# Optimization experiments

Measured on AMD Instinct MI355X. Metric: run time of the kernel, lower is better.

## Reference

```python
import jax, jax.numpy as jnp
import numpy as np

T, B, N, D, H = 12, 32, 64, 2, 128
HID, HEAD = 32, 4          # GATBlock n_hid, n_head; HEAD*HID == H
M = N * (N - 1)            # edge rows per get_graph
N_ACT = N - 1              # active nodes per batch row


def _make_graph():
    rec = np.zeros((M, N), np.float32)
    snd = np.zeros((M, N), np.float32)
    k = np.arange(N_ACT * N_ACT)
    ii = np.repeat(np.arange(N_ACT), N_ACT)
    jj = np.tile(np.arange(N_ACT), N_ACT)
    snd[k, ii] = 1.0
    rec[k, jj] = 1.0
    return rec, snd


def setup_inputs() -> dict:
    key = jax.random.key(0)
    ks = jax.random.split(key, 16)
    rec, snd = _make_graph()
    inp = {
        "inputs": jax.random.normal(ks[0], (T, B, N, D), jnp.float32),
        "hidden": jax.random.normal(ks[1], (B, N, H), jnp.float32),
        "rel_rec": jnp.asarray(np.broadcast_to(rec, (B, M, N)).copy()),
        "rel_send": jnp.asarray(np.broadcast_to(snd, (B, M, N)).copy()),
        # GATBlock rn1: fc1(D->HID), fc2(2*HID->HEAD)
        "rn1_W1": jax.random.normal(ks[2], (HID, D)) * 0.1,
        "rn1_b1": jnp.zeros((HID,)),
        "rn1_W2": jax.random.normal(ks[3], (HEAD, 2 * HID)) * 0.1,
        "rn1_b2": jnp.zeros((HEAD,)),
        # GATBlock rn2: fc1(H->HID), fc2(2*HID->HEAD)
        "rn2_W1": jax.random.normal(ks[4], (HID, H)) * 0.1,
        "rn2_b1": jnp.zeros((HID,)),
        "rn2_W2": jax.random.normal(ks[5], (HEAD, 2 * HID)) * 0.1,
        "rn2_b2": jnp.zeros((HEAD,)),
        # GRUCell(H, H)
        "gru_Wih": jax.random.normal(ks[6], (3 * H, H)) * 0.05,
        "gru_Whh": jax.random.normal(ks[7], (3 * H, H)) * 0.05,
        "gru_bih": jnp.zeros((3 * H,)),
        "gru_bhh": jnp.zeros((3 * H,)),
        # out Linear(H, D)
        "out_W": jax.random.normal(ks[8], (D, H)) * 0.1,
        "out_b": jnp.zeros((D,)),
    }
    return inp


def _gat_block(x_in, rel_rec, rel_send, W1, b1, W2, b2):
    # x_in: B x N x Din
    x = x_in @ W1.T + b1                                   # B,N,HID
    s = jnp.einsum('bmn,bnd->bmd', rel_send, x)            # B,M,HID (senders)
    r = jnp.einsum('bmn,bnd->bmd', rel_rec, x)             # B,M,HID (receivers)
    a = jax.nn.elu(jnp.concatenate([s, r], -1) @ W2.T + b2)  # B,M,HEAD
    # per-receiving-node masked softmax over the edge dim (edge2node)
    m = rel_rec[..., None] > 0                             # B,M,N,1
    logits = jnp.where(m, a[:, :, None, :], -jnp.inf)      # B,M,N,HEAD
    mx = jnp.max(logits, axis=1, keepdims=True)
    mx = jnp.where(jnp.isfinite(mx), mx, 0.0)
    e = jnp.where(m, jnp.exp(logits - mx), 0.0)
    denom = jnp.sum(e, axis=1, keepdims=True)
    att = e / jnp.where(denom > 0, denom, 1.0)             # B,M,N,HEAD
    # weighted scatter-sum: outer(att_edge, sender_feat) summed per node
    out = jnp.einsum('bmnh,bmd->bnhd', att, s)             # B,N,HEAD,HID
    Bn, Nn = x_in.shape[0], x_in.shape[1]
    return jax.nn.elu(out.reshape(Bn, Nn, HEAD * HID))     # B,N,H


def _gru_cell(x, h, Wih, Whh, bih, bhh):
    gi = x @ Wih.T + bih
    gh = h @ Whh.T + bhh
    i_r, i_z, i_n = jnp.split(gi, 3, axis=-1)
    h_r, h_z, h_n = jnp.split(gh, 3, axis=-1)
    r = jax.nn.sigmoid(i_r + h_r)
    z = jax.nn.sigmoid(i_z + h_z)
    n = jnp.tanh(i_n + r * h_n)
    return (1.0 - z) * n + z * h


def reference(inputs, hidden, rel_rec, rel_send,
              rn1_W1, rn1_b1, rn1_W2, rn1_b2,
              rn2_W1, rn2_b1, rn2_W2, rn2_b2,
              gru_Wih, gru_Whh, gru_bih, gru_bhh,
              out_W, out_b):
    def step(h, x_t):
        x = _gat_block(x_t, rel_rec, rel_send, rn1_W1, rn1_b1, rn1_W2, rn1_b2)
        h = _gru_cell(x, h, gru_Wih, gru_Whh, gru_bih, gru_bhh)
        h = _gat_block(h, rel_rec, rel_send, rn2_W1, rn2_b1, rn2_W2, rn2_b2)
        return h, None
    h_final, _ = jax.lax.scan(step, hidden, inputs)
    pred = h_final @ out_W.T + out_b                       # B,N,D
    return pred
```

## Files before the change

kernel.cpp:

```cpp
#include <hip/hip_runtime.h>


#define T_   12
#define B_   32
#define N_   64
#define D_   2
#define H_   128
#define HID_ 32
#define HEAD_ 4
#define NA_  63

__device__ __forceinline__ float eluf(float x){ return x>0.f ? x : expm1f(x); }

#define OFF_H    0u
#define OFF_X1   262144u
#define OFF_PS1  1048576u
#define OFF_PR1  1146880u
#define OFF_XG   1245184u
#define OFF_X2   4390912u
#define OFF_PS2  4456448u
#define OFF_PR2  4464640u
#define OFF_WT   OFF_X1
#define OFF_GI   4472832u
#define WS_NEED_A ((4472832ull + 9437184ull) * 4ull)

__global__ void gat1_fc(const float* __restrict__ inp, const float* __restrict__ W1,
                        const float* __restrict__ b1, const float* __restrict__ W2,
                        const float* __restrict__ b2,
                        float* __restrict__ x1_all, float* __restrict__ ps_all,
                        float* __restrict__ pr_all){
  int grp = blockIdx.x;
  int tid = threadIdx.x;
  __shared__ float sx1[N_*HID_];
  __shared__ float sW1[HID_*D_];
  __shared__ float sb1[HID_];
  __shared__ float sW2[HEAD_*2*HID_];
  __shared__ float sxin[N_*D_];
  if(tid < 64)  sW1[tid] = W1[tid];
  if(tid < 32)  sb1[tid] = b1[tid];
  sW2[tid] = W2[tid];
  if(tid < 128) sxin[tid] = inp[grp*N_*D_ + tid];
  __syncthreads();
  for(int o = tid; o < N_*HID_; o += 256){
    int n = o >> 5, k = o & 31;
    float v = sb1[k] + sxin[n*2]*sW1[k*2] + sxin[n*2+1]*sW1[k*2+1];
    sx1[o] = v;
    x1_all[grp*N_*HID_ + o] = v;
  }
  __syncthreads();
  for(int p = tid; p < N_*8; p += 256){
    int n = p >> 3, q = p & 7, hh = q & 3;
    const float* w  = sW2 + hh*64 + ((q < 4) ? 0 : 32);
    const float* xr = sx1 + n*32;
    float acc = (q < 4) ? b2[hh] : 0.f;
    #pragma unroll
    for(int c = 0; c < 32; c++) acc += xr[c]*w[c];
    if(q < 4) ps_all[grp*N_*HEAD_ + n*4 + hh] = acc;
    else      pr_all[grp*N_*HEAD_ + n*4 + hh] = acc;
  }
}

__global__ void prep_wt(const float* __restrict__ Wih, const float* __restrict__ Whh,
                        float* __restrict__ wtb){
  int idx = blockIdx.x*256 + threadIdx.x;
  int k4 = idx / 768, j = idx - k4*768;
  const float* src = (j < 384) ? (Wih + (size_t)j*H_) : (Whh + (size_t)(j-384)*H_);
  ((float4*)wtb)[idx] = ((const float4*)src)[k4];
}

__global__ __launch_bounds__(128) void gat_att_big(const float* __restrict__ x1,
    const float* __restrict__ ps, const float* __restrict__ pr,
    float* __restrict__ out){
  int blk = blockIdx.x, g = blk >> 1, part = blk & 1, tid = threadIdx.x;
  __shared__ float sX[N_*HID_];
  __shared__ float sPs[N_*HEAD_];
  __shared__ float sPr[N_*HEAD_];
  {
    const float4* xs = (const float4*)(x1 + (size_t)g*(N_*HID_));
    #pragma unroll
    for(int k = 0; k < 4; k++) ((float4*)sX)[tid + 128*k] = xs[tid + 128*k];
    sPs[tid]       = ps[g*(N_*HEAD_) + tid];
    sPs[tid + 128] = ps[g*(N_*HEAD_) + tid + 128];
    sPr[tid]       = pr[g*(N_*HEAD_) + tid];
    sPr[tid + 128] = pr[g*(N_*HEAD_) + tid + 128];
  }
  __syncthreads();
  float* outg = out + (size_t)g*(N_*H_);
  int r = part*128 + tid;
  if(r < NA_*HEAD_){
    int hh = r & 3;
    float prv = sPr[r];
    float tmax = -1e30f;
    for(int i = 0; i < NA_; i++) tmax = fmaxf(tmax, sPs[i*4 + hh]);
    float m = eluf(tmax + prv);
    float4 acc[8];
    #pragma unroll
    for(int k = 0; k < 8; k++) acc[k] = make_float4(0.f,0.f,0.f,0.f);
    float s = 0.f;
    #pragma unroll 3
    for(int i = 0; i < NA_; i++){
      float tt = sPs[i*4 + hh] + prv;
      float v = tt > 0.f ? tt : expm1f(tt);
      float p = expf(v - m);
      s += p;
      const float4* sxp = (const float4*)&sX[i*32];
      #pragma unroll
      for(int k = 0; k < 8; k++){
        float4 xv = sxp[k];
        acc[k].x += p*xv.x; acc[k].y += p*xv.y;
        acc[k].z += p*xv.z; acc[k].w += p*xv.w;
      }
    }
    float inv = 1.f/s;
    float4* orow = (float4*)(outg + (r>>2)*H_ + hh*32);
    #pragma unroll
    for(int k = 0; k < 8; k++){
      float4 o;
      o.x = eluf(acc[k].x*inv); o.y = eluf(acc[k].y*inv);
      o.z = eluf(acc[k].z*inv); o.w = eluf(acc[k].w*inv);
      orow[k] = o;
    }
  } else {
    float4 z4 = make_float4(0.f,0.f,0.f,0.f);
    float4* zrow = (float4*)(outg + NA_*H_);
    for(int k = r - NA_*HEAD_; k < 32; k += 4) zrow[k] = z4;
  }
}

__global__ __launch_bounds__(192) void gi_gemm2(const float* __restrict__ xg,
    const float* __restrict__ wtb, float* __restrict__ gi){
  int tid = threadIdx.x;
  int r0 = blockIdx.x * 8;
  __shared__ __align__(16) float sxg[8][H_];
  for(int i = tid; i < 256; i += 192)
    ((float4*)sxg)[i] = ((const float4*)(xg + (size_t)r0*H_))[i];
  __syncthreads();
  const float4* wt4 = (const float4*)wtb;
  float acc0[8] = {0,0,0,0,0,0,0,0};
  float acc1[8] = {0,0,0,0,0,0,0,0};
  #pragma unroll 4
  for(int k4 = 0; k4 < 32; k4++){
    float4 w0 = wt4[k4*768 + tid];
    float4 w1 = wt4[k4*768 + tid + 192];
    #pragma unroll
    for(int rr = 0; rr < 8; rr++){
      float4 xv = ((const float4*)sxg[rr])[k4];
      acc0[rr] += w0.x*xv.x + w0.y*xv.y + w0.z*xv.z + w0.w*xv.w;
      acc1[rr] += w1.x*xv.x + w1.y*xv.y + w1.z*xv.z + w1.w*xv.w;
    }
  }
  #pragma unroll
  for(int rr = 0; rr < 8; rr++){
    gi[(size_t)(r0+rr)*384 + tid]       = acc0[rr];
    gi[(size_t)(r0+rr)*384 + tid + 192] = acc1[rr];
  }
}

__global__ __launch_bounds__(512) void gru_fc4(
    const float* __restrict__ gi, const float* __restrict__ h,
    const float* __restrict__ wtb,
    const float* __restrict__ bih, const float* __restrict__ bhh,
    const float* __restrict__ W1, const float* __restrict__ b1,
    const float* __restrict__ W2, const float* __restrict__ b2,
    float* __restrict__ x2, float* __restrict__ ps2, float* __restrict__ pr2){
  int tid = threadIdx.x;
  int g0 = blockIdx.x * 8;
  __shared__ __align__(16) float sh[8][H_];
  __shared__ __align__(16) float shn[8][H_];
  __shared__ float sx2[8][HID_];
  if(tid < 256) ((float4*)sh)[tid] = ((const float4*)(h + (size_t)g0*H_))[tid];
  __syncthreads();
  int c = tid & 127, rg = tid >> 7, r0 = rg*2;
  const float4* wt4 = (const float4*)wtb;
  const float4* hp0 = (const float4*)sh[r0];
  const float4* hp1 = (const float4*)sh[r0+1];
  float ahr[2]={0,0}, ahz[2]={0,0}, ahn[2]={0,0};
  #pragma unroll 4
  for(int k4 = 0; k4 < 32; k4++){
    const float4* wk = wt4 + k4*768 + c;
    float4 w3 = wk[384], w4 = wk[512], w5 = wk[640];
    float4 hv0 = hp0[k4], hv1 = hp1[k4];
    ahr[0] += w3.x*hv0.x + w3.y*hv0.y + w3.z*hv0.z + w3.w*hv0.w;
    ahz[0] += w4.x*hv0.x + w4.y*hv0.y + w4.z*hv0.z + w4.w*hv0.w;
    ahn[0] += w5.x*hv0.x + w5.y*hv0.y + w5.z*hv0.z + w5.w*hv0.w;
    ahr[1] += w3.x*hv1.x + w3.y*hv1.y + w3.z*hv1.z + w3.w*hv1.w;
    ahz[1] += w4.x*hv1.x + w4.y*hv1.y + w4.z*hv1.z + w4.w*hv1.w;
    ahn[1] += w5.x*hv1.x + w5.y*hv1.y + w5.z*hv1.z + w5.w*hv1.w;
  }
  float bi_r = bih[c], bi_z = bih[c+H_], bi_n = bih[c+2*H_];
  float bh_r = bhh[c], bh_z = bhh[c+H_], bh_n = bhh[c+2*H_];
  #pragma unroll
  for(int rr = 0; rr < 2; rr++){
    const float* gir = gi + (size_t)(g0+r0+rr)*384;
    float ir  = gir[c]       + bi_r;
    float iz  = gir[c+128]   + bi_z;
    float in_ = gir[c+256]   + bi_n;
    float hr  = ahr[rr]+bh_r, hz = ahz[rr]+bh_z, hn = ahn[rr]+bh_n;
    float rgt = 1.f/(1.f+expf(-(ir+hr)));
    float zgt = 1.f/(1.f+expf(-(iz+hz)));
    float ngt = tanhf(in_ + rgt*hn);
    shn[r0+rr][c] = (1.f-zgt)*ngt + zgt*sh[r0+rr][c];
  }
  __syncthreads();
  if(tid < 256){
    int r = tid >> 5, jc = tid & 31;
    const float4* wrow = (const float4*)(W1 + (size_t)jc*H_);
    const float4* hnr = (const float4*)shn[r];
    float acc = b1[jc];
    #pragma unroll 8
    for(int k4 = 0; k4 < 32; k4++){
      float4 w = wrow[k4], hv = hnr[k4];
      acc += w.x*hv.x + w.y*hv.y + w.z*hv.z + w.w*hv.w;
    }
    sx2[r][jc] = acc;
    x2[(size_t)(g0+r)*HID_ + jc] = acc;
  }
  __syncthreads();
  if(tid < 64){
    int r = tid >> 3, q = tid & 7, hh = q & 3;
    int base = (q < 4) ? 0 : 32;
    float acc = (q < 4) ? b2[hh] : 0.f;
    #pragma unroll
    for(int cc = 0; cc < 32; cc++) acc += sx2[r][cc]*W2[hh*64 + base + cc];
    if(q < 4) ps2[(g0+r)*HEAD_ + hh] = acc;
    else      pr2[(g0+r)*HEAD_ + hh] = acc;
  }
}

__global__ __launch_bounds__(512) void gru_fc3(
    const float* __restrict__ xg, const float* __restrict__ h,
    const float* __restrict__ wtb,
    const float* __restrict__ bih, const float* __restrict__ bhh,
    const float* __restrict__ W1, const float* __restrict__ b1,
    const float* __restrict__ W2, const float* __restrict__ b2,
    float* __restrict__ x2, float* __restrict__ ps2, float* __restrict__ pr2){
  int tid = threadIdx.x;
  int g0 = blockIdx.x * 8;
  __shared__ __align__(16) float sx[8][H_];
  __shared__ __align__(16) float sh[8][H_];
  __shared__ __align__(16) float shn[8][H_];
  __shared__ float sx2[8][HID_];
  if(tid < 256) ((float4*)sx)[tid]     = ((const float4*)(xg + (size_t)g0*H_))[tid];
  else          ((float4*)sh)[tid-256] = ((const float4*)(h  + (size_t)g0*H_))[tid-256];
  __syncthreads();
  int c = tid & 127, rg = tid >> 7, r0 = rg*2;
  const float4* wt4 = (const float4*)wtb;
  const float4* xr0 = (const float4*)sx[r0];
  const float4* xr1 = (const float4*)sx[r0+1];
  const float4* hp0 = (const float4*)sh[r0];
  const float4* hp1 = (const float4*)sh[r0+1];
  float air[2]={0,0}, aiz[2]={0,0}, ain[2]={0,0};
  float ahr[2]={0,0}, ahz[2]={0,0}, ahn[2]={0,0};
  #pragma unroll 2
  for(int k4 = 0; k4 < 32; k4++){
    const float4* wk = wt4 + k4*768 + c;
    float4 w0 = wk[0],   w1 = wk[128], w2 = wk[256];
    float4 w3 = wk[384], w4 = wk[512], w5 = wk[640];
    float4 xv0 = xr0[k4], xv1 = xr1[k4];
    float4 hv0 = hp0[k4], hv1 = hp1[k4];
    air[0] += w0.x*xv0.x + w0.y*xv0.y + w0.z*xv0.z + w0.w*xv0.w;
    aiz[0] += w1.x*xv0.x + w1.y*xv0.y + w1.z*xv0.z + w1.w*xv0.w;
    ain[0] += w2.x*xv0.x + w2.y*xv0.y + w2.z*xv0.z + w2.w*xv0.w;
    ahr[0] += w3.x*hv0.x + w3.y*hv0.y + w3.z*hv0.z + w3.w*hv0.w;
    ahz[0] += w4.x*hv0.x + w4.y*hv0.y + w4.z*hv0.z + w4.w*hv0.w;
    ahn[0] += w5.x*hv0.x + w5.y*hv0.y + w5.z*hv0.z + w5.w*hv0.w;
    air[1] += w0.x*xv1.x + w0.y*xv1.y + w0.z*xv1.z + w0.w*xv1.w;
    aiz[1] += w1.x*xv1.x + w1.y*xv1.y + w1.z*xv1.z + w1.w*xv1.w;
    ain[1] += w2.x*xv1.x + w2.y*xv1.y + w2.z*xv1.z + w2.w*xv1.w;
    ahr[1] += w3.x*hv1.x + w3.y*hv1.y + w3.z*hv1.z + w3.w*hv1.w;
    ahz[1] += w4.x*hv1.x + w4.y*hv1.y + w4.z*hv1.z + w4.w*hv1.w;
    ahn[1] += w5.x*hv1.x + w5.y*hv1.y + w5.z*hv1.z + w5.w*hv1.w;
  }
  float bi_r = bih[c], bi_z = bih[c+H_], bi_n = bih[c+2*H_];
  float bh_r = bhh[c], bh_z = bhh[c+H_], bh_n = bhh[c+2*H_];
  #pragma unroll
  for(int rr = 0; rr < 2; rr++){
    float ir  = air[rr]+bi_r, iz = aiz[rr]+bi_z, in_ = ain[rr]+bi_n;
    float hr  = ahr[rr]+bh_r, hz = ahz[rr]+bh_z, hn  = ahn[rr]+bh_n;
    float rgt = 1.f/(1.f+expf(-(ir+hr)));
    float zgt = 1.f/(1.f+expf(-(iz+hz)));
    float ngt = tanhf(in_ + rgt*hn);
    shn[r0+rr][c] = (1.f-zgt)*ngt + zgt*sh[r0+rr][c];
  }
  __syncthreads();
  if(tid < 256){
    int r = tid >> 5, jc = tid & 31;
    const float4* wrow = (const float4*)(W1 + (size_t)jc*H_);
    const float4* hnr = (const float4*)shn[r];
    float acc = b1[jc];
    #pragma unroll 8
    for(int k4 = 0; k4 < 32; k4++){
      float4 w = wrow[k4], hv = hnr[k4];
      acc += w.x*hv.x + w.y*hv.y + w.z*hv.z + w.w*hv.w;
    }
    sx2[r][jc] = acc;
    x2[(size_t)(g0+r)*HID_ + jc] = acc;
  }
  __syncthreads();
  if(tid < 64){
    int r = tid >> 3, q = tid & 7, hh = q & 3;
    int base = (q < 4) ? 0 : 32;
    float acc = (q < 4) ? b2[hh] : 0.f;
    #pragma unroll
    for(int cc = 0; cc < 32; cc++) acc += sx2[r][cc]*W2[hh*64 + base + cc];
    if(q < 4) ps2[(g0+r)*HEAD_ + hh] = acc;
    else      pr2[(g0+r)*HEAD_ + hh] = acc;
  }
}

__global__ __launch_bounds__(128) void gat_att_sm(const float* __restrict__ x1,
    const float* __restrict__ ps, const float* __restrict__ pr,
    float* __restrict__ out){
  int bid = blockIdx.x;
  int g = bid >> 3, sub = bid & 7, rh = sub >> 2, dq = sub & 3;
  int tid = threadIdx.x;
  __shared__ float sX[N_*HID_];
  __shared__ float sPs[N_*HEAD_];
  __shared__ float sPr[N_*HEAD_];
  {
    const float4* xs = (const float4*)(x1 + (size_t)g*(N_*HID_));
    #pragma unroll
    for(int k = 0; k < 4; k++) ((float4*)sX)[tid + 128*k] = xs[tid + 128*k];
    sPs[tid]       = ps[g*(N_*HEAD_) + tid];
    sPs[tid + 128] = ps[g*(N_*HEAD_) + tid + 128];
    sPr[tid]       = pr[g*(N_*HEAD_) + tid];
    sPr[tid + 128] = pr[g*(N_*HEAD_) + tid + 128];
  }
  __syncthreads();
  float* outg = out + (size_t)g*(N_*H_);
  if(tid < 126){
    int r = rh*126 + tid;
    int hh = r & 3, j = r >> 2;
    float prv = sPr[r];
    float tmax = -1e30f;
    for(int i = 0; i < NA_; i++) tmax = fmaxf(tmax, sPs[i*4 + hh]);
    float m = eluf(tmax + prv);
    float4 a0 = make_float4(0.f,0.f,0.f,0.f), a1 = a0;
    float s = 0.f;
    #pragma unroll 3
    for(int i = 0; i < NA_; i++){
      float tt = sPs[i*4 + hh] + prv;
      float v = tt > 0.f ? tt : expm1f(tt);
      float p = expf(v - m);
      s += p;
      const float4* sxp = (const float4*)&sX[i*32 + dq*8];
      float4 x0 = sxp[0], x1v = sxp[1];
      a0.x += p*x0.x;  a0.y += p*x0.y;  a0.z += p*x0.z;  a0.w += p*x0.w;
      a1.x += p*x1v.x; a1.y += p*x1v.y; a1.z += p*x1v.z; a1.w += p*x1v.w;
    }
    float inv = 1.f/s;
    float4* orow = (float4*)(outg + (size_t)j*H_ + hh*32 + dq*8);
    float4 o0, o1;
    o0.x = eluf(a0.x*inv); o0.y = eluf(a0.y*inv);
    o0.z = eluf(a0.z*inv); o0.w = eluf(a0.w*inv);
    o1.x = eluf(a1.x*inv); o1.y = eluf(a1.y*inv);
    o1.z = eluf(a1.z*inv); o1.w = eluf(a1.w*inv);
    orow[0] = o0; orow[1] = o1;
  } else if(rh == 1){
    float4 z4 = make_float4(0.f,0.f,0.f,0.f);
    float4* zrow = (float4*)(outg + NA_*H_);
    int base = dq*8 + (tid-126)*4;
    #pragma unroll
    for(int k = 0; k < 4; k++) zrow[base + k] = z4;
  }
}

__global__ void final_k(const float* __restrict__ h, const float* __restrict__ oW,
                        const float* __restrict__ ob, float* __restrict__ out){
  int b = blockIdx.x, tid = threadIdx.x;
  int n = tid >> 1, d = tid & 1;
  const float* hr = h + (size_t)(b*N_ + n)*H_;
  float acc = ob[d];
  #pragma unroll 8
  for(int k = 0; k < H_; k++) acc += hr[k]*oW[d*H_ + k];
  out[(b*N_ + n)*D_ + d] = acc;
}

extern "C" void kernel_launch(void* const* d_in, const int* in_sizes, int n_in,
                              void* d_out, int out_size, void* d_ws, size_t ws_size,
                              hipStream_t stream){
  const float* inputs = (const float*)d_in[0];
  const float* hidden = (const float*)d_in[1];
  const float* rn1_W1 = (const float*)d_in[4];
  const float* rn1_b1 = (const float*)d_in[5];
  const float* rn1_W2 = (const float*)d_in[6];
  const float* rn1_b2 = (const float*)d_in[7];
  const float* rn2_W1 = (const float*)d_in[8];
  const float* rn2_b1 = (const float*)d_in[9];
  const float* rn2_W2 = (const float*)d_in[10];
  const float* rn2_b2 = (const float*)d_in[11];
  const float* gWih   = (const float*)d_in[12];
  const float* gWhh   = (const float*)d_in[13];
  const float* gbih   = (const float*)d_in[14];
  const float* gbhh   = (const float*)d_in[15];
  const float* oW     = (const float*)d_in[16];
  const float* ob     = (const float*)d_in[17];
  float* ws = (float*)d_ws;

  const int use_gi = (ws_size >= WS_NEED_A) ? 1 : 0;

  gat1_fc<<<T_*B_, 256, 0, stream>>>(inputs, rn1_W1, rn1_b1, rn1_W2, rn1_b2,
                                     ws + OFF_X1, ws + OFF_PS1, ws + OFF_PR1);
  gat_att_big<<<T_*B_*2, 128, 0, stream>>>(ws + OFF_X1, ws + OFF_PS1, ws + OFF_PR1,
                                           ws + OFF_XG);
  prep_wt<<<96, 256, 0, stream>>>(gWih, gWhh, ws + OFF_WT);

  const float* xg0  = ws + OFF_XG;
  const float* wtbp = ws + OFF_WT;
  float* hb  = ws + OFF_H;
  float* x2p = ws + OFF_X2;
  float* psp = ws + OFF_PS2;
  float* prp = ws + OFF_PR2;

  if(use_gi){
    gi_gemm2<<<T_*B_*N_/8, 192, 0, stream>>>(xg0, wtbp, ws + OFF_GI);
  }
  for(int t = 0; t < T_; t++){
    const float* hsrc = (t == 0) ? hidden : hb;
    if(use_gi){
      gru_fc4<<<B_*N_/8, 512, 0, stream>>>(ws + OFF_GI + (size_t)t*B_*N_*384, hsrc,
                                           wtbp, gbih, gbhh,
                                           rn2_W1, rn2_b1, rn2_W2, rn2_b2,
                                           x2p, psp, prp);
    } else {
      gru_fc3<<<B_*N_/8, 512, 0, stream>>>(xg0 + (size_t)t*B_*N_*H_, hsrc,
                                           wtbp, gbih, gbhh,
                                           rn2_W1, rn2_b1, rn2_W2, rn2_b2,
                                           x2p, psp, prp);
    }
    gat_att_sm<<<B_*8, 128, 0, stream>>>(x2p, psp, prp, hb);
  }
  final_k<<<B_, 128, 0, stream>>>(hb, oW, ob, (float*)d_out);
}
```

Before: 558.9 us.

## Fuse GAT attention into GRU step kernel with ping-pong buffers

Each step's GRU kernel now recomputes the rn2 attention from the previous step's x2/ps/pr buffers, so the per-step gat_att_sm launch disappears and only one kernel runs per timestep, with ping-pong buffers reusing freed workspace regions. The hidden-hidden matvec is restructured to split K across four row groups, each computing all 8 rows, with a shared-memory reduction. The input-gate GEMM tile doubles to 16 rows per block. The costs are redundant softmax work across the 8 blocks per batch, more shared memory per block, and higher register pressure.

```diff
diff --git a/kernel.cpp b/kernel.cpp
--- a/kernel.cpp
+++ b/kernel.cpp
@@ -127,81 +127,137 @@
   }
 }
 
-__global__ __launch_bounds__(192) void gi_gemm2(const float* __restrict__ xg,
+__global__ __launch_bounds__(192) void gi_gemm3(const float* __restrict__ xg,
     const float* __restrict__ wtb, float* __restrict__ gi){
   int tid = threadIdx.x;
-  int r0 = blockIdx.x * 8;
-  __shared__ __align__(16) float sxg[8][H_];
-  for(int i = tid; i < 256; i += 192)
+  int r0 = blockIdx.x * 16;
+  __shared__ __align__(16) float sxg[16][H_];
+  for(int i = tid; i < 512; i += 192)
     ((float4*)sxg)[i] = ((const float4*)(xg + (size_t)r0*H_))[i];
   __syncthreads();
   const float4* wt4 = (const float4*)wtb;
-  float acc0[8] = {0,0,0,0,0,0,0,0};
-  float acc1[8] = {0,0,0,0,0,0,0,0};
-  #pragma unroll 4
+  float acc0[16] = {0,0,0,0,0,0,0,0,0,0,0,0,0,0,0,0};
+  float acc1[16] = {0,0,0,0,0,0,0,0,0,0,0,0,0,0,0,0};
+  #pragma unroll 2
   for(int k4 = 0; k4 < 32; k4++){
     float4 w0 = wt4[k4*768 + tid];
     float4 w1 = wt4[k4*768 + tid + 192];
     #pragma unroll
-    for(int rr = 0; rr < 8; rr++){
+    for(int rr = 0; rr < 16; rr++){
       float4 xv = ((const float4*)sxg[rr])[k4];
       acc0[rr] += w0.x*xv.x + w0.y*xv.y + w0.z*xv.z + w0.w*xv.w;
       acc1[rr] += w1.x*xv.x + w1.y*xv.y + w1.z*xv.z + w1.w*xv.w;
     }
   }
   #pragma unroll
-  for(int rr = 0; rr < 8; rr++){
+  for(int rr = 0; rr < 16; rr++){
     gi[(size_t)(r0+rr)*384 + tid]       = acc0[rr];
     gi[(size_t)(r0+rr)*384 + tid + 192] = acc1[rr];
   }
 }
 
-__global__ __launch_bounds__(512) void gru_fc4(
-    const float* __restrict__ gi, const float* __restrict__ h,
+__global__ __launch_bounds__(512) void gru_fc5(
+    const float* __restrict__ gi, const float* __restrict__ hidden0, int t0,
+    const float* __restrict__ x2prev, const float* __restrict__ psprev,
+    const float* __restrict__ prprev,
     const float* __restrict__ wtb,
     const float* __restrict__ bih, const float* __restrict__ bhh,
     const float* __restrict__ W1, const float* __restrict__ b1,
     const float* __restrict__ W2, const float* __restrict__ b2,
     float* __restrict__ x2, float* __restrict__ ps2, float* __restrict__ pr2){
-  int tid = threadIdx.x;
-  int g0 = blockIdx.x * 8;
+  int tid = threadIdx.x, blk = blockIdx.x;
+  int g0 = blk*8, g = blk>>3, jbase = (blk&7)*8;
+  __shared__ __align__(16) float sX[N_*HID_];
+  __shared__ float sPs[N_*HEAD_];
   __shared__ __align__(16) float sh[8][H_];
   __shared__ __align__(16) float shn[8][H_];
+  __shared__ float spart[4][24][H_];
   __shared__ float sx2[8][HID_];
-  if(tid < 256) ((float4*)sh)[tid] = ((const float4*)(h + (size_t)g0*H_))[tid];
-  __syncthreads();
-  int c = tid & 127, rg = tid >> 7, r0 = rg*2;
-  const float4* wt4 = (const float4*)wtb;
-  const float4* hp0 = (const float4*)sh[r0];
-  const float4* hp1 = (const float4*)sh[r0+1];
-  float ahr[2]={0,0}, ahz[2]={0,0}, ahn[2]={0,0};
-  #pragma unroll 4
-  for(int k4 = 0; k4 < 32; k4++){
-    const float4* wk = wt4 + k4*768 + c;
-    float4 w3 = wk[384], w4 = wk[512], w5 = wk[640];
-    float4 hv0 = hp0[k4], hv1 = hp1[k4];
-    ahr[0] += w3.x*hv0.x + w3.y*hv0.y + w3.z*hv0.z + w3.w*hv0.w;
-    ahz[0] += w4.x*hv0.x + w4.y*hv0.y + w4.z*hv0.z + w4.w*hv0.w;
-    ahn[0] += w5.x*hv0.x + w5.y*hv0.y + w5.z*hv0.z + w5.w*hv0.w;
-    ahr[1] += w3.x*hv1.x + w3.y*hv1.y + w3.z*hv1.z + w3.w*hv1.w;
-    ahz[1] += w4.x*hv1.x + w4.y*hv1.y + w4.z*hv1.z + w4.w*hv1.w;
-    ahn[1] += w5.x*hv1.x + w5.y*hv1.y + w5.z*hv1.z + w5.w*hv1.w;
-  }
-  float bi_r = bih[c], bi_z = bih[c+H_], bi_n = bih[c+2*H_];
-  float bh_r = bhh[c], bh_z = bhh[c+H_], bh_n = bhh[c+2*H_];
-  #pragma unroll
-  for(int rr = 0; rr < 2; rr++){
-    const float* gir = gi + (size_t)(g0+r0+rr)*384;
-    float ir  = gir[c]       + bi_r;
-    float iz  = gir[c+128]   + bi_z;
-    float in_ = gir[c+256]   + bi_n;
-    float hr  = ahr[rr]+bh_r, hz = ahz[rr]+bh_z, hn = ahn[rr]+bh_n;
-    float rgt = 1.f/(1.f+expf(-(ir+hr)));
-    float zgt = 1.f/(1.f+expf(-(iz+hz)));
-    float ngt = tanhf(in_ + rgt*hn);
-    shn[r0+rr][c] = (1.f-zgt)*ngt + zgt*sh[r0+rr][c];
-  }
-  __syncthreads();
+
+  if(t0){
+    if(tid < 256) ((float4*)sh)[tid] = ((const float4*)(hidden0 + (size_t)g0*H_))[tid];
+  } else {
+    ((float4*)sX)[tid] = ((const float4*)(x2prev + (size_t)g*(N_*HID_)))[tid];
+    if(tid < 256) sPs[tid] = psprev[g*(N_*HEAD_) + tid];
+  }
+  __syncthreads();
+
+  if(!t0){
+    int rl = tid >> 4, l16 = tid & 15;
+    int hh = rl & 3, jrow = rl >> 2;
+    int jl = jbase + jrow;
+    float prv = prprev[g*(N_*HEAD_) + jbase*4 + rl];
+    float tmax = -1e30f;
+    for(int i = 0; i < NA_; i++) tmax = fmaxf(tmax, sPs[i*4 + hh]);
+    float m = eluf(tmax + prv);
+    float a0 = 0.f, a1 = 0.f, s = 0.f;
+    #pragma unroll 3
+    for(int i = 0; i < NA_; i++){
+      float tt = sPs[i*4 + hh] + prv;
+      float v = tt > 0.f ? tt : expm1f(tt);
+      float p = expf(v - m);
+      s += p;
+      const float2 xv = *(const float2*)&sX[i*32 + l16*2];
+      a0 += p*xv.x; a1 += p*xv.y;
+    }
+    float inv = 1.f/s;
+    float h0 = (jl == NA_) ? 0.f : eluf(a0*inv);
+    float h1 = (jl == NA_) ? 0.f : eluf(a1*inv);
+    sh[jrow][hh*32 + l16*2]     = h0;
+    sh[jrow][hh*32 + l16*2 + 1] = h1;
+  }
+  __syncthreads();
+
+  int c = tid & 127, rg = tid >> 7;
+  {
+    const float4* wt4 = (const float4*)wtb;
+    float ar[8] = {0,0,0,0,0,0,0,0};
+    float az[8] = {0,0,0,0,0,0,0,0};
+    float an[8] = {0,0,0,0,0,0,0,0};
+    #pragma unroll
+    for(int kk = 0; kk < 8; kk++){
+      int k4 = rg*8 + kk;
+      const float4* wk = wt4 + (size_t)k4*768 + 384 + c;
+      float4 wr_ = wk[0], wz_ = wk[128], wn_ = wk[256];
+      #pragma unroll
+      for(int r = 0; r < 8; r++){
+        float4 hv = ((const float4*)sh[r])[k4];
+        ar[r] += wr_.x*hv.x + wr_.y*hv.y + wr_.z*hv.z + wr_.w*hv.w;
+        az[r] += wz_.x*hv.x + wz_.y*hv.y + wz_.z*hv.z + wz_.w*hv.w;
+        an[r] += wn_.x*hv.x + wn_.y*hv.y + wn_.z*hv.z + wn_.w*hv.w;
+      }
+    }
+    #pragma unroll
+    for(int r = 0; r < 8; r++){
+      spart[rg][r][c]      = ar[r];
+      spart[rg][8 + r][c]  = az[r];
+      spart[rg][16 + r][c] = an[r];
+    }
+  }
+  __syncthreads();
+
+  {
+    float bi_r = bih[c], bi_z = bih[c+H_], bi_n = bih[c+2*H_];
+    float bh_r = bhh[c], bh_z = bhh[c+H_], bh_n = bhh[c+2*H_];
+    int r0 = rg*2;
+    #pragma unroll
+    for(int rr = 0; rr < 2; rr++){
+      int r = r0 + rr;
+      float hr = spart[0][r][c] + spart[1][r][c] + spart[2][r][c] + spart[3][r][c] + bh_r;
+      float hz = spart[0][8+r][c] + spart[1][8+r][c] + spart[2][8+r][c] + spart[3][8+r][c] + bh_z;
+      float hn = spart[0][16+r][c] + spart[1][16+r][c] + spart[2][16+r][c] + spart[3][16+r][c] + bh_n;
+      const float* gir = gi + (size_t)(g0+r)*384;
+      float ir  = gir[c]     + bi_r;
+      float iz  = gir[c+128] + bi_z;
+      float in_ = gir[c+256] + bi_n;
+      float rgt = 1.f/(1.f+expf(-(ir+hr)));
+      float zgt = 1.f/(1.f+expf(-(iz+hz)));
+      float ngt = tanhf(in_ + rgt*hn);
+      shn[r][c] = (1.f-zgt)*ngt + zgt*sh[r][c];
+    }
+  }
+  __syncthreads();
+
   if(tid < 256){
     int r = tid >> 5, jc = tid & 31;
     const float4* wrow = (const float4*)(W1 + (size_t)jc*H_);
@@ -408,27 +464,34 @@
   const float* xg0  = ws + OFF_XG;
   const float* wtbp = ws + OFF_WT;
   float* hb  = ws + OFF_H;
-  float* x2p = ws + OFF_X2;
-  float* psp = ws + OFF_PS2;
-  float* prp = ws + OFF_PR2;
 
   if(use_gi){
-    gi_gemm2<<<T_*B_*N_/8, 192, 0, stream>>>(xg0, wtbp, ws + OFF_GI);
-  }
-  for(int t = 0; t < T_; t++){
-    const float* hsrc = (t == 0) ? hidden : hb;
-    if(use_gi){
-      gru_fc4<<<B_*N_/8, 512, 0, stream>>>(ws + OFF_GI + (size_t)t*B_*N_*384, hsrc,
-                                           wtbp, gbih, gbhh,
-                                           rn2_W1, rn2_b1, rn2_W2, rn2_b2,
-                                           x2p, psp, prp);
-    } else {
+    gi_gemm3<<<T_*B_*N_/16, 192, 0, stream>>>(xg0, wtbp, ws + OFF_GI);
+    float* x2b[2] = {ws + OFF_X2,  ws + OFF_PS1};
+    float* psb[2] = {ws + OFF_PS2, ws + OFF_PR1};
+    float* prb[2] = {ws + OFF_PR2, ws + OFF_PR1 + 8192};
+    for(int t = 0; t < T_; t++){
+      int w = t & 1, rp = w ^ 1;
+      gru_fc5<<<256, 512, 0, stream>>>(ws + OFF_GI + (size_t)t*B_*N_*384,
+                                       hidden, (t == 0) ? 1 : 0,
+                                       x2b[rp], psb[rp], prb[rp],
+                                       wtbp, gbih, gbhh,
+                                       rn2_W1, rn2_b1, rn2_W2, rn2_b2,
+                                       x2b[w], psb[w], prb[w]);
+    }
+    gat_att_sm<<<B_*8, 128, 0, stream>>>(x2b[1], psb[1], prb[1], hb);
+  } else {
+    float* x2p = ws + OFF_X2;
+    float* psp = ws + OFF_PS2;
+    float* prp = ws + OFF_PR2;
+    for(int t = 0; t < T_; t++){
+      const float* hsrc = (t == 0) ? hidden : hb;
       gru_fc3<<<B_*N_/8, 512, 0, stream>>>(xg0 + (size_t)t*B_*N_*H_, hsrc,
                                            wtbp, gbih, gbhh,
                                            rn2_W1, rn2_b1, rn2_W2, rn2_b2,
                                            x2p, psp, prp);
-    }
-    gat_att_sm<<<B_*8, 128, 0, stream>>>(x2p, psp, prp, hb);
+      gat_att_sm<<<B_*8, 128, 0, stream>>>(x2p, psp, prp, hb);
+    }
   }
   final_k<<<B_, 128, 0, stream>>>(hb, oW, ob, (float*)d_out);
 }
```

New measurement: 470.4 us. -15.8%, faster.
